# Optimization experiments

Measured on AMD Instinct MI355X. Metric: run time of the kernel, lower is better.

Reference implementation:

```python
import jax, jax.numpy as jnp
import numpy as np

B, L, C = 4, 1024, 768
H = 12
D = C // H  # head_dim = 64


def setup_inputs() -> dict:
    key = jax.random.key(0)
    k_x, k_qkv, k_pw, k_pb = jax.random.split(key, 4)
    x = jax.random.normal(k_x, (B, L, C), dtype=jnp.float32)
    # torch nn.Linear(C, 3C, bias=False): weight [3C, C]
    w_qkv = jax.random.normal(k_qkv, (3 * C, C), dtype=jnp.float32) * (1.0 / np.sqrt(C))
    # torch nn.Linear(C, C): weight [C, C], bias [C]
    w_proj = jax.random.normal(k_pw, (C, C), dtype=jnp.float32) * (1.0 / np.sqrt(C))
    b_proj = jax.random.normal(k_pb, (C,), dtype=jnp.float32) * 0.01
    return {"x": x, "w_qkv": w_qkv, "w_proj": w_proj, "b_proj": b_proj}


def reference(x, w_qkv, w_proj, b_proj):
    scale = D ** (-0.5)
    # qkv: [B, L, 3C] -> [3, B, H, L, D]
    qkv = jnp.einsum('blc,fc->blf', x, w_qkv)
    qkv = qkv.reshape(B, L, 3, H, D).transpose(2, 0, 3, 1, 4)
    q, k, v = qkv[0], qkv[1], qkv[2]
    # attention scores [B, H, L, L], materialized (returned by the module)
    attn = jnp.einsum('bhld,bhmd->bhlm', q, k) * scale
    attn_score = jax.nn.softmax(attn, axis=-1)
    # dropout_p = 0.0 -> identity
    out = jnp.einsum('bhlm,bhmd->bhld', attn_score, v)
    out = out.transpose(0, 2, 1, 3).reshape(B, L, C)
    out = jnp.einsum('blc,fc->blf', out, w_proj) + b_proj
    return (out, attn_score)
```

## Files before the change

### kernel.cpp

```cpp
#include <hip/hip_runtime.h>
#include <hip/hip_bf16.h>
#include <stdint.h>


typedef __attribute__((ext_vector_type(8))) short short8;
typedef __attribute__((ext_vector_type(4))) float floatx4;

#define MFMA16(A_, B_, C_) __builtin_amdgcn_mfma_f32_16x16x32_bf16((A_), (B_), (C_), 0, 0, 0)

__device__ __forceinline__ unsigned short f2bf(float f) {
  unsigned u = __builtin_bit_cast(unsigned, f);
  u += 0x7FFFu + ((u >> 16) & 1u);
  return (unsigned short)(u >> 16);
}
__device__ __forceinline__ float bf2f(unsigned short u) {
  return __builtin_bit_cast(float, (unsigned)u << 16);
}

__global__ __launch_bounds__(256) void cast_kernel(const float* __restrict__ src,
                                                   unsigned short* __restrict__ dst, int n) {
  int i = (blockIdx.x * 256 + threadIdx.x) * 4;
  if (i < n) {
    float4 v = *(const float4*)(src + i);
    ushort4 o;
    o.x = f2bf(v.x); o.y = f2bf(v.y); o.z = f2bf(v.z); o.w = f2bf(v.w);
    *(ushort4*)(dst + i) = o;
  }
}

template <int EPI>
__global__ __launch_bounds__(256) void gemm_bt(
    const unsigned short* __restrict__ A, const unsigned short* __restrict__ Bm,
    const float* __restrict__ bias,
    unsigned short* __restrict__ q_ws, unsigned short* __restrict__ k_ws,
    unsigned short* __restrict__ vt_ws, float* __restrict__ Cout,
    int M, int N, int K) {
  __shared__ __align__(16) unsigned short Al[128 * 32];
  __shared__ __align__(16) unsigned short Bl[128 * 32];
  const int tid = threadIdx.x;
  const int lane = tid & 63, wave = tid >> 6;
  const int q = lane >> 4, lm = lane & 15;
  const int wm = wave >> 1, wn = wave & 1;
  const int m0 = blockIdx.y * 128, n0 = blockIdx.x * 128;

  floatx4 acc[4][4];
#pragma unroll
  for (int i = 0; i < 4; ++i)
#pragma unroll
    for (int j = 0; j < 4; ++j) acc[i][j] = (floatx4){0.f, 0.f, 0.f, 0.f};

  for (int k0 = 0; k0 < K; k0 += 32) {
#pragma unroll
    for (int it = 0; it < 2; ++it) {
      int idx = tid + it * 256;
      int row = idx >> 2, ch = idx & 3;
      const unsigned short* ga = A + (size_t)(m0 + row) * K + k0 + ch * 8;
      const unsigned short* gb = Bm + (size_t)(n0 + row) * K + k0 + ch * 8;
      __builtin_amdgcn_global_load_lds(
          (const __attribute__((address_space(1))) unsigned int*)ga,
          (__attribute__((address_space(3))) unsigned int*)(Al + idx * 8), 16, 0, 0);
      __builtin_amdgcn_global_load_lds(
          (const __attribute__((address_space(1))) unsigned int*)gb,
          (__attribute__((address_space(3))) unsigned int*)(Bl + idx * 8), 16, 0, 0);
    }
    __syncthreads();
    short8 af[4], bfr[4];
#pragma unroll
    for (int t = 0; t < 4; ++t) {
      af[t] = *(const short8*)(Al + (wm * 64 + t * 16 + lm) * 32 + q * 8);
      bfr[t] = *(const short8*)(Bl + (wn * 64 + t * 16 + lm) * 32 + q * 8);
    }
#pragma unroll
    for (int i = 0; i < 4; ++i)
#pragma unroll
      for (int j = 0; j < 4; ++j) acc[i][j] = MFMA16(af[i], bfr[j], acc[i][j]);
    __syncthreads();
  }

  if (EPI == 0) {
#pragma unroll
    for (int i = 0; i < 4; ++i) {
      int mb = m0 + wm * 64 + i * 16 + q * 4;
#pragma unroll
      for (int j = 0; j < 4; ++j) {
        int n = n0 + wn * 64 + j * 16 + lm;
        int which = n / 768;
        int r = n - which * 768;
        int h = r >> 6, d = r & 63;
#pragma unroll
        for (int rg = 0; rg < 4; ++rg) {
          int m = mb + rg;
          int b = m >> 10, l = m & 1023;
          float v = acc[i][j][rg];
          if (which == 0) v *= 0.125f;
          unsigned short bv = f2bf(v);
          if (which == 0)
            q_ws[(size_t)((b * 12 + h) * 1024 + l) * 64 + d] = bv;
          else if (which == 1)
            k_ws[(size_t)((b * 12 + h) * 1024 + l) * 64 + d] = bv;
          else
            vt_ws[(size_t)((b * 12 + h) * 64 + d) * 1024 + l] = bv;
        }
      }
    }
  } else {
#pragma unroll
    for (int i = 0; i < 4; ++i) {
      int mb = m0 + wm * 64 + i * 16 + q * 4;
#pragma unroll
      for (int j = 0; j < 4; ++j) {
        int n = n0 + wn * 64 + j * 16 + lm;
        float bv = bias[n];
#pragma unroll
        for (int rg = 0; rg < 4; ++rg) {
          int m = mb + rg;
          Cout[(size_t)m * N + n] = acc[i][j][rg] + bv;
        }
      }
    }
  }
}

__global__ __launch_bounds__(256) void attn_mfma(
    const unsigned short* __restrict__ q_ws, const unsigned short* __restrict__ k_ws,
    const unsigned short* __restrict__ vt_ws, unsigned short* __restrict__ attn_o,
    float* __restrict__ out1) {
  constexpr int L = 1024, SW = 1034;
  __shared__ __align__(16) unsigned short S[16 * SW];
  __shared__ float sinv[16];
  const int bh = blockIdx.y, b = bh / 12, h = bh % 12;
  const int l0 = blockIdx.x * 16;
  const int tid = threadIdx.x, lane = tid & 63, wave = tid >> 6;
  const int q = lane >> 4, lm = lane & 15;

  const size_t qk_base = (size_t)bh * L * 64;

  const unsigned short* qr = q_ws + qk_base + (size_t)(l0 + lm) * 64;
  short8 aq0 = *(const short8*)(qr + q * 8);
  short8 aq1 = *(const short8*)(qr + 32 + q * 8);

#pragma unroll 2
  for (int ct = wave * 16; ct < wave * 16 + 16; ++ct) {
    const unsigned short* kr = k_ws + qk_base + (size_t)(ct * 16 + lm) * 64;
    short8 b0 = *(const short8*)(kr + q * 8);
    short8 b1 = *(const short8*)(kr + 32 + q * 8);
    floatx4 acc = (floatx4){0.f, 0.f, 0.f, 0.f};
    acc = MFMA16(aq0, b0, acc);
    acc = MFMA16(aq1, b1, acc);
#pragma unroll
    for (int rg = 0; rg < 4; ++rg)
      S[(q * 4 + rg) * SW + ct * 16 + lm] = f2bf(acc[rg]);
  }
  __syncthreads();

  {
    int r = tid >> 4, j = tid & 15;
    unsigned short* Sr = S + r * SW;
    float mx = -1e30f;
    for (int m = j; m < L; m += 16) mx = fmaxf(mx, bf2f(Sr[m]));
#pragma unroll
    for (int off = 1; off < 16; off <<= 1) mx = fmaxf(mx, __shfl_xor(mx, off, 16));
    float sum = 0.f;
    for (int m = j; m < L; m += 16) {
      float e = __expf(bf2f(Sr[m]) - mx);
      sum += e;
      Sr[m] = f2bf(e);
    }
#pragma unroll
    for (int off = 1; off < 16; off <<= 1) sum += __shfl_xor(sum, off, 16);
    if (j == 0) sinv[r] = 1.0f / sum;
  }
  __syncthreads();

  {
    size_t ob = (size_t)bh * L * L + (size_t)l0 * L;
    for (int idx = tid; idx < 16 * L; idx += 256) {
      int r = idx >> 10, m = idx & (L - 1);
      out1[ob + (size_t)r * L + m] = bf2f(S[r * SW + m]) * sinv[r];
    }
  }

  {
    floatx4 acc = (floatx4){0.f, 0.f, 0.f, 0.f};
    const unsigned short* vr = vt_ws + (size_t)(bh * 64 + wave * 16 + lm) * 1024;
#pragma unroll 4
    for (int ks = 0; ks < 32; ++ks) {
      const unsigned short* sp = S + lm * SW + ks * 32 + q * 8;
      union { unsigned u[4]; short8 s8; } af;
      af.u[0] = *(const unsigned*)(sp + 0);
      af.u[1] = *(const unsigned*)(sp + 2);
      af.u[2] = *(const unsigned*)(sp + 4);
      af.u[3] = *(const unsigned*)(sp + 6);
      short8 bv = *(const short8*)(vr + ks * 32 + q * 8);
      acc = MFMA16(af.s8, bv, acc);
    }
#pragma unroll
    for (int rg = 0; rg < 4; ++rg) {
      int row = q * 4 + rg;
      float v = acc[rg] * sinv[row];
      attn_o[(size_t)(b * 1024 + l0 + row) * 768 + h * 64 + wave * 16 + lm] = f2bf(v);
    }
  }
}

extern "C" void kernel_launch(void* const* d_in, const int* in_sizes, int n_in,
                              void* d_out, int out_size, void* d_ws, size_t ws_size,
                              hipStream_t stream) {
  const float* x      = (const float*)d_in[0];
  const float* w_qkv  = (const float*)d_in[1];
  const float* w_proj = (const float*)d_in[2];
  const float* b_proj = (const float*)d_in[3];

  float* out0 = (float*)d_out;
  float* out1 = out0 + (size_t)4096 * 768;

  const size_t NX = (size_t)4096 * 768;
  const size_t NWQ = (size_t)2304 * 768;
  const size_t NWP = (size_t)768 * 768;
  const size_t NQ = (size_t)48 * 1024 * 64;

  unsigned short* x_bf   = (unsigned short*)d_ws;
  unsigned short* wq_bf  = x_bf + NX;
  unsigned short* wp_bf  = wq_bf + NWQ;
  unsigned short* q_ws   = wp_bf + NWP;
  unsigned short* k_ws   = q_ws + NQ;
  unsigned short* vt_ws  = k_ws + NQ;
  unsigned short* attn_o = vt_ws + NQ;

  cast_kernel<<<dim3(NX / 1024), dim3(256), 0, stream>>>(x, x_bf, (int)NX);
  cast_kernel<<<dim3(NWQ / 1024), dim3(256), 0, stream>>>(w_qkv, wq_bf, (int)NWQ);
  cast_kernel<<<dim3(NWP / 1024), dim3(256), 0, stream>>>(w_proj, wp_bf, (int)NWP);

  gemm_bt<0><<<dim3(2304 / 128, 4096 / 128), dim3(256), 0, stream>>>(
      x_bf, wq_bf, nullptr, q_ws, k_ws, vt_ws, nullptr, 4096, 2304, 768);

  attn_mfma<<<dim3(64, 48), dim3(256), 0, stream>>>(q_ws, k_ws, vt_ws, attn_o, out1);

  gemm_bt<1><<<dim3(768 / 128, 4096 / 128), dim3(256), 0, stream>>>(
      attn_o, wp_bf, b_proj, nullptr, nullptr, nullptr, out0, 4096, 768, 768);
}
```

Before: 379.7 us.

## Keep attention scores in registers for softmax, fuse casts, vectorize V-transpose stores

The attention kernel swaps the MFMA operand order so each lane holds four consecutive columns of one row. Scores then stay in registers in fp32 for the max/sum reductions, with cross-wave stats exchanged through small shared arrays. The normalized probabilities are written as float4 to the output and as packed bf16 to shared memory for the PV MFMA, which removes the serial LDS softmax pass and the strided scalar output loop. The three cast launches are merged into one, and V-transpose stores in the QKV GEMM epilogue are packed into ushort4. The change costs more registers (16 floatx4 accumulators per lane) and drops the LDS row padding from 1034 to 1032 elements, which may add bank conflicts.

```diff
diff --git a/kernel.cpp b/kernel.cpp
--- a/kernel.cpp
+++ b/kernel.cpp
@@ -17,15 +17,21 @@
   return __builtin_bit_cast(float, (unsigned)u << 16);
 }
 
-__global__ __launch_bounds__(256) void cast_kernel(const float* __restrict__ src,
-                                                   unsigned short* __restrict__ dst, int n) {
+__global__ __launch_bounds__(256) void cast3_kernel(const float* __restrict__ x,
+                                                    const float* __restrict__ wq,
+                                                    const float* __restrict__ wp,
+                                                    unsigned short* __restrict__ dst) {
+  const int NX = 3145728, NWQ = 1769472;
   int i = (blockIdx.x * 256 + threadIdx.x) * 4;
-  if (i < n) {
-    float4 v = *(const float4*)(src + i);
-    ushort4 o;
-    o.x = f2bf(v.x); o.y = f2bf(v.y); o.z = f2bf(v.z); o.w = f2bf(v.w);
-    *(ushort4*)(dst + i) = o;
-  }
+  const float* src;
+  int off;
+  if (i < NX) { src = x; off = i; }
+  else if (i < NX + NWQ) { src = wq; off = i - NX; }
+  else { src = wp; off = i - NX - NWQ; }
+  float4 v = *(const float4*)(src + off);
+  ushort4 o;
+  o.x = f2bf(v.x); o.y = f2bf(v.y); o.z = f2bf(v.z); o.w = f2bf(v.w);
+  *(ushort4*)(dst + i) = o;
 }
 
 template <int EPI>
@@ -87,19 +93,23 @@
         int which = n / 768;
         int r = n - which * 768;
         int h = r >> 6, d = r & 63;
-#pragma unroll
-        for (int rg = 0; rg < 4; ++rg) {
-          int m = mb + rg;
-          int b = m >> 10, l = m & 1023;
-          float v = acc[i][j][rg];
-          if (which == 0) v *= 0.125f;
-          unsigned short bv = f2bf(v);
-          if (which == 0)
-            q_ws[(size_t)((b * 12 + h) * 1024 + l) * 64 + d] = bv;
-          else if (which == 1)
-            k_ws[(size_t)((b * 12 + h) * 1024 + l) * 64 + d] = bv;
-          else
-            vt_ws[(size_t)((b * 12 + h) * 64 + d) * 1024 + l] = bv;
+        if (which == 2) {
+          int b = mb >> 10, l = mb & 1023;
+          ushort4 pk;
+          pk.x = f2bf(acc[i][j][0]);
+          pk.y = f2bf(acc[i][j][1]);
+          pk.z = f2bf(acc[i][j][2]);
+          pk.w = f2bf(acc[i][j][3]);
+          *(ushort4*)(vt_ws + (size_t)((b * 12 + h) * 64 + d) * 1024 + l) = pk;
+        } else {
+          unsigned short* dst = (which == 0) ? q_ws : k_ws;
+          float sc = (which == 0) ? 0.125f : 1.0f;
+#pragma unroll
+          for (int rg = 0; rg < 4; ++rg) {
+            int m = mb + rg;
+            int b = m >> 10, l = m & 1023;
+            dst[(size_t)((b * 12 + h) * 1024 + l) * 64 + d] = f2bf(acc[i][j][rg] * sc);
+          }
         }
       }
     }
@@ -125,9 +135,9 @@
     const unsigned short* __restrict__ q_ws, const unsigned short* __restrict__ k_ws,
     const unsigned short* __restrict__ vt_ws, unsigned short* __restrict__ attn_o,
     float* __restrict__ out1) {
-  constexpr int L = 1024, SW = 1034;
+  constexpr int L = 1024, SW = 1032;
   __shared__ __align__(16) unsigned short S[16 * SW];
-  __shared__ float sinv[16];
+  __shared__ float stats[2][4][16];
   const int bh = blockIdx.y, b = bh / 12, h = bh % 12;
   const int l0 = blockIdx.x * 16;
   const int tid = threadIdx.x, lane = tid & 63, wave = tid >> 6;
@@ -136,69 +146,77 @@
   const size_t qk_base = (size_t)bh * L * 64;
 
   const unsigned short* qr = q_ws + qk_base + (size_t)(l0 + lm) * 64;
-  short8 aq0 = *(const short8*)(qr + q * 8);
-  short8 aq1 = *(const short8*)(qr + 32 + q * 8);
-
-#pragma unroll 2
-  for (int ct = wave * 16; ct < wave * 16 + 16; ++ct) {
-    const unsigned short* kr = k_ws + qk_base + (size_t)(ct * 16 + lm) * 64;
-    short8 b0 = *(const short8*)(kr + q * 8);
-    short8 b1 = *(const short8*)(kr + 32 + q * 8);
-    floatx4 acc = (floatx4){0.f, 0.f, 0.f, 0.f};
-    acc = MFMA16(aq0, b0, acc);
-    acc = MFMA16(aq1, b1, acc);
-#pragma unroll
-    for (int rg = 0; rg < 4; ++rg)
-      S[(q * 4 + rg) * SW + ct * 16 + lm] = f2bf(acc[rg]);
-  }
+  short8 bq0 = *(const short8*)(qr + q * 8);
+  short8 bq1 = *(const short8*)(qr + 32 + q * 8);
+
+  floatx4 acc[16];
+#pragma unroll
+  for (int ct = 0; ct < 16; ++ct) {
+    const unsigned short* kr = k_ws + qk_base + (size_t)((wave * 16 + ct) * 16 + lm) * 64;
+    short8 a0 = *(const short8*)(kr + q * 8);
+    short8 a1 = *(const short8*)(kr + 32 + q * 8);
+    floatx4 c = (floatx4){0.f, 0.f, 0.f, 0.f};
+    c = MFMA16(a0, bq0, c);
+    c = MFMA16(a1, bq1, c);
+    acc[ct] = c;
+  }
+
+  float mloc = -1e30f;
+#pragma unroll
+  for (int ct = 0; ct < 16; ++ct)
+#pragma unroll
+    for (int rg = 0; rg < 4; ++rg) mloc = fmaxf(mloc, acc[ct][rg]);
+  mloc = fmaxf(mloc, __shfl_xor(mloc, 16));
+  mloc = fmaxf(mloc, __shfl_xor(mloc, 32));
+  if (lane < 16) stats[0][wave][lane] = mloc;
   __syncthreads();
+  float m = fmaxf(fmaxf(stats[0][0][lm], stats[0][1][lm]),
+                  fmaxf(stats[0][2][lm], stats[0][3][lm]));
+
+  float ssum = 0.f;
+#pragma unroll
+  for (int ct = 0; ct < 16; ++ct) {
+#pragma unroll
+    for (int rg = 0; rg < 4; ++rg) {
+      float e = exp2f((acc[ct][rg] - m) * 1.44269504f);
+      acc[ct][rg] = e;
+      ssum += e;
+    }
+  }
+  ssum += __shfl_xor(ssum, 16);
+  ssum += __shfl_xor(ssum, 32);
+  if (lane < 16) stats[1][wave][lane] = ssum;
+  __syncthreads();
+  float sinv = 1.0f / (stats[1][0][lm] + stats[1][1][lm] + stats[1][2][lm] + stats[1][3][lm]);
+
+  float* orow = out1 + (size_t)bh * L * L + (size_t)(l0 + lm) * L + wave * 256 + q * 4;
+  unsigned short* srow = S + lm * SW + wave * 256 + q * 4;
+#pragma unroll
+  for (int ct = 0; ct < 16; ++ct) {
+    float p0 = acc[ct][0] * sinv, p1 = acc[ct][1] * sinv;
+    float p2 = acc[ct][2] * sinv, p3 = acc[ct][3] * sinv;
+    ushort4 pk;
+    pk.x = f2bf(p0); pk.y = f2bf(p1); pk.z = f2bf(p2); pk.w = f2bf(p3);
+    *(ushort4*)(srow + ct * 16) = pk;
+    float4 pv;
+    pv.x = p0; pv.y = p1; pv.z = p2; pv.w = p3;
+    *(float4*)(orow + ct * 16) = pv;
+  }
+  __syncthreads();
 
   {
-    int r = tid >> 4, j = tid & 15;
-    unsigned short* Sr = S + r * SW;
-    float mx = -1e30f;
-    for (int m = j; m < L; m += 16) mx = fmaxf(mx, bf2f(Sr[m]));
-#pragma unroll
-    for (int off = 1; off < 16; off <<= 1) mx = fmaxf(mx, __shfl_xor(mx, off, 16));
-    float sum = 0.f;
-    for (int m = j; m < L; m += 16) {
-      float e = __expf(bf2f(Sr[m]) - mx);
-      sum += e;
-      Sr[m] = f2bf(e);
-    }
-#pragma unroll
-    for (int off = 1; off < 16; off <<= 1) sum += __shfl_xor(sum, off, 16);
-    if (j == 0) sinv[r] = 1.0f / sum;
-  }
-  __syncthreads();
-
-  {
-    size_t ob = (size_t)bh * L * L + (size_t)l0 * L;
-    for (int idx = tid; idx < 16 * L; idx += 256) {
-      int r = idx >> 10, m = idx & (L - 1);
-      out1[ob + (size_t)r * L + m] = bf2f(S[r * SW + m]) * sinv[r];
-    }
-  }
-
-  {
-    floatx4 acc = (floatx4){0.f, 0.f, 0.f, 0.f};
+    floatx4 pacc = (floatx4){0.f, 0.f, 0.f, 0.f};
     const unsigned short* vr = vt_ws + (size_t)(bh * 64 + wave * 16 + lm) * 1024;
 #pragma unroll 4
     for (int ks = 0; ks < 32; ++ks) {
-      const unsigned short* sp = S + lm * SW + ks * 32 + q * 8;
-      union { unsigned u[4]; short8 s8; } af;
-      af.u[0] = *(const unsigned*)(sp + 0);
-      af.u[1] = *(const unsigned*)(sp + 2);
-      af.u[2] = *(const unsigned*)(sp + 4);
-      af.u[3] = *(const unsigned*)(sp + 6);
+      short8 af = *(const short8*)(S + lm * SW + ks * 32 + q * 8);
       short8 bv = *(const short8*)(vr + ks * 32 + q * 8);
-      acc = MFMA16(af.s8, bv, acc);
+      pacc = MFMA16(af, bv, pacc);
     }
 #pragma unroll
     for (int rg = 0; rg < 4; ++rg) {
       int row = q * 4 + rg;
-      float v = acc[rg] * sinv[row];
-      attn_o[(size_t)(b * 1024 + l0 + row) * 768 + h * 64 + wave * 16 + lm] = f2bf(v);
+      attn_o[(size_t)(b * 1024 + l0 + row) * 768 + h * 64 + wave * 16 + lm] = f2bf(pacc[rg]);
     }
   }
 }
@@ -227,9 +245,7 @@
   unsigned short* vt_ws  = k_ws + NQ;
   unsigned short* attn_o = vt_ws + NQ;
 
-  cast_kernel<<<dim3(NX / 1024), dim3(256), 0, stream>>>(x, x_bf, (int)NX);
-  cast_kernel<<<dim3(NWQ / 1024), dim3(256), 0, stream>>>(w_qkv, wq_bf, (int)NWQ);
-  cast_kernel<<<dim3(NWP / 1024), dim3(256), 0, stream>>>(w_proj, wp_bf, (int)NWP);
+  cast3_kernel<<<dim3((NX + NWQ + NWP) / 1024), dim3(256), 0, stream>>>(x, w_qkv, w_proj, x_bf);
 
   gemm_bt<0><<<dim3(2304 / 128, 4096 / 128), dim3(256), 0, stream>>>(
       x_bf, wq_bf, nullptr, q_ws, k_ws, vt_ws, nullptr, 4096, 2304, 768);
```

Result: faster. 359.3 us (-5.4%).
